# Kernel tuning notes

Measured on AMD Instinct MI355X. Metric: run time of the kernel, lower is better.

Reference implementation:

```python
import jax, jax.numpy as jnp
import numpy as np
import math

HEAD_DIM = 64
N_Q = 64
N_KV = 8
HIDDEN = 2880
SLIDING = 128
BASE = 150000.0
INIT_CTX = 4096
SCALE = 32.0
NTK_A = 1.0
NTK_B = 32.0
SEQ = 2048


def _rope_cos_sin(position_ids):
    # YaRN-scaled inverse frequencies (scaling_factor > 1 branch)
    freq = BASE ** (jnp.arange(0, HEAD_DIM, 2, dtype=jnp.float32) / HEAD_DIM)
    concentration = 0.1 * math.log(SCALE) + 1.0
    d_half = HEAD_DIM // 2
    low = d_half * math.log(INIT_CTX / (NTK_B * 2 * math.pi)) / math.log(BASE)
    high = d_half * math.log(INIT_CTX / (NTK_A * 2 * math.pi)) / math.log(BASE)
    interpolation = 1.0 / (SCALE * freq)
    extrapolation = 1.0 / freq
    ramp = (jnp.arange(d_half, dtype=jnp.float32) - low) / (high - low)
    mask = 1.0 - jnp.clip(ramp, 0.0, 1.0)
    inv_freq = interpolation * (1.0 - mask) + extrapolation * mask
    freqs = position_ids.astype(jnp.float32)[:, None] * inv_freq[None, :]  # [n, d/2]
    return jnp.cos(freqs) * concentration, jnp.sin(freqs) * concentration


def _apply_rope(x, cos, sin):
    # x: [n, h, d]; cos/sin: [n, d/2]
    cos = cos[:, None, :].astype(x.dtype)
    sin = sin[:, None, :].astype(x.dtype)
    x1, x2 = jnp.split(x, 2, axis=-1)
    return jnp.concatenate([x1 * cos - x2 * sin, x2 * cos + x1 * sin], axis=-1)


def setup_inputs() -> dict:
    key = jax.random.key(0)
    ks = jax.random.split(key, 6)
    qkv_dim = HEAD_DIM * (N_Q + 2 * N_KV)
    return {
        "hidden_states": jax.random.normal(ks[0], (SEQ, HIDDEN), dtype=jnp.float32),
        "qkv_w": jax.random.normal(ks[1], (qkv_dim, HIDDEN), dtype=jnp.float32) * 0.02,
        "qkv_b": jax.random.normal(ks[2], (qkv_dim,), dtype=jnp.float32) * 0.02,
        "o_w": jax.random.normal(ks[3], (HIDDEN, N_Q * HEAD_DIM), dtype=jnp.float32) * 0.02,
        "o_b": jax.random.normal(ks[4], (HIDDEN,), dtype=jnp.float32) * 0.02,
        "sinks": jax.random.normal(ks[5], (N_Q,), dtype=jnp.float32),
        "position_ids": jnp.arange(SEQ, dtype=jnp.int64 if jax.config.jax_enable_x64 else jnp.int32),
    }


def reference(hidden_states, qkv_w, qkv_b, o_w, o_b, sinks, position_ids):
    n = hidden_states.shape[0]
    scaling = HEAD_DIM ** (-0.5)

    # fused QKV projection + split
    qkv = hidden_states @ qkv_w.T + qkv_b  # [n, (nq+2*nkv)*d]
    q_sz, k_sz = N_Q * HEAD_DIM, N_KV * HEAD_DIM
    q = qkv[:, :q_sz].reshape(n, N_Q, HEAD_DIM)
    k = qkv[:, q_sz:q_sz + k_sz].reshape(n, N_KV, HEAD_DIM)
    v = qkv[:, q_sz + k_sz:].reshape(n, N_KV, HEAD_DIM)

    # RoPE (YaRN)
    cos, sin = _rope_cos_sin(position_ids)
    q = _apply_rope(q, cos, sin)
    k = _apply_rope(k, cos, sin)

    # GQA: repeat KV heads to match query heads
    groups = N_Q // N_KV
    k_full = jnp.repeat(k, groups, axis=1)  # [n, N_Q, d]
    v_full = jnp.repeat(v, groups, axis=1)

    scores = jnp.einsum('qhd,khd->hqk', q, k_full) * scaling  # [H, S, S]

    # sliding-window mask (distance > window -> -inf), as in source (no causal term)
    current_pos = position_ids.max()
    key_pos = current_pos - n + 1 + jnp.arange(n)
    dist = position_ids[:, None] - key_pos[None, :]
    win_mask = jnp.where(dist > SLIDING, -jnp.inf, 0.0).astype(scores.dtype)
    scores = scores + win_mask[None, :, :]

    # learned sink logit appended to softmax normalization
    sink = jnp.broadcast_to(sinks[:, None, None], (N_Q, n, 1)).astype(scores.dtype)
    logits = jnp.concatenate([scores, sink], axis=-1)  # [H, S, S+1]
    probs = jax.nn.softmax(logits, axis=-1)[..., :-1]   # drop sink column

    attn = jnp.einsum('hqk,khd->qhd', probs, v_full)    # [S, H, d]
    attn = attn.reshape(n, N_Q * HEAD_DIM)
    return attn @ o_w.T + o_b
```

## Files before the change

kernel.cpp:

```cpp
#include <hip/hip_runtime.h>
#include <hip/hip_bf16.h>
#include <stdint.h>

typedef __attribute__((ext_vector_type(4))) float f32x4;
typedef __attribute__((ext_vector_type(8))) short bf16x8;

#define SEQ 2048
#define HIDDEN 2880
#define NQ 64
#define NKV 8
#define HD 64
#define QKV_DIM 5120
#define Q_SZ 4096
#define K_SZ 512
#define OW_N 2880
#define OW_NPAD 2944
#define OW_K 4096

__device__ __forceinline__ unsigned short f2b_bits(float f) {
    unsigned int x = __float_as_uint(f);
    unsigned int r = (x + 0x7fffu + ((x >> 16) & 1u)) >> 16;
    return (unsigned short)r;
}
__device__ __forceinline__ float b2f(unsigned short u) {
    return __uint_as_float(((unsigned int)u) << 16);
}

__device__ __forceinline__ void llds16(const ushort* g, ushort* l) {
    __builtin_amdgcn_global_load_lds(
        (const __attribute__((address_space(1))) void*)g,
        (__attribute__((address_space(3))) void*)l, 16, 0, 0);
}

__global__ void convert_f32(const float* __restrict__ in, ushort* __restrict__ out, int n4) {
    int i = blockIdx.x * blockDim.x + threadIdx.x;
    int stride = gridDim.x * blockDim.x;
    for (; i < n4; i += stride) {
        float4 v = reinterpret_cast<const float4*>(in)[i];
        ushort4 o = make_ushort4(f2b_bits(v.x), f2b_bits(v.y), f2b_bits(v.z), f2b_bits(v.w));
        reinterpret_cast<ushort4*>(out)[i] = o;
    }
}

__global__ void convert_ow(const float* __restrict__ in, ushort* __restrict__ out) {
    int i = blockIdx.x * blockDim.x + threadIdx.x;
    const int n4 = OW_NPAD * OW_K / 4;
    int stride = gridDim.x * blockDim.x;
    for (; i < n4; i += stride) {
        int row = (i * 4) >> 12;
        ushort4 o;
        if (row < OW_N) {
            float4 v = reinterpret_cast<const float4*>(in)[i];
            o = make_ushort4(f2b_bits(v.x), f2b_bits(v.y), f2b_bits(v.z), f2b_bits(v.w));
        } else {
            o = make_ushort4(0, 0, 0, 0);
        }
        reinterpret_cast<ushort4*>(out)[i] = o;
    }
}

template<int OUT_BF16>
__global__ __launch_bounds__(256) void gemm_bt(
    const ushort* __restrict__ A, const ushort* __restrict__ B,
    const float* __restrict__ bias, void* __restrict__ Cout,
    int M, int N, int K, int Nreal, int ldC)
{
    __shared__ __align__(16) ushort As[128 * 64];
    __shared__ __align__(16) ushort Bs[128 * 64];
    const int tid = threadIdx.x;
    const int lane = tid & 63;
    const int w = tid >> 6;
    const int wr = w >> 1, wc = w & 1;
    const int m0 = blockIdx.y * 128, n0 = blockIdx.x * 128;

    f32x4 acc[4][4] = {};

    for (int k0 = 0; k0 < K; k0 += 64) {
        #pragma unroll
        for (int it = 0; it < 4; ++it) {
            int i = it * 256 + tid;
            int row = i >> 3;
            int col16 = (i ^ (row & 7)) & 7;
            const ushort* ga = A + (size_t)(m0 + row) * K + k0 + col16 * 8;
            ushort* la = As + (size_t)(it * 256 + (tid & ~63)) * 8;
            llds16(ga, la);
            const ushort* gb = B + (size_t)(n0 + row) * K + k0 + col16 * 8;
            ushort* lb = Bs + (size_t)(it * 256 + (tid & ~63)) * 8;
            llds16(gb, lb);
        }
        __syncthreads();
        #pragma unroll
        for (int kk = 0; kk < 2; ++kk) {
            bf16x8 a[4], b[4];
            #pragma unroll
            for (int mi = 0; mi < 4; ++mi) {
                int row = wr * 64 + mi * 16 + (lane & 15);
                int byte = row * 128 + kk * 64 + (lane >> 4) * 16;
                byte ^= (row & 7) << 4;
                a[mi] = *reinterpret_cast<const bf16x8*>(reinterpret_cast<const char*>(As) + byte);
            }
            #pragma unroll
            for (int ni = 0; ni < 4; ++ni) {
                int row = wc * 64 + ni * 16 + (lane & 15);
                int byte = row * 128 + kk * 64 + (lane >> 4) * 16;
                byte ^= (row & 7) << 4;
                b[ni] = *reinterpret_cast<const bf16x8*>(reinterpret_cast<const char*>(Bs) + byte);
            }
            #pragma unroll
            for (int mi = 0; mi < 4; ++mi)
                #pragma unroll
                for (int ni = 0; ni < 4; ++ni)
                    acc[mi][ni] = __builtin_amdgcn_mfma_f32_16x16x32_bf16(a[mi], b[ni], acc[mi][ni], 0, 0, 0);
        }
        __syncthreads();
    }

    #pragma unroll
    for (int mi = 0; mi < 4; ++mi) {
        int gr = m0 + wr * 64 + mi * 16 + (lane >> 4) * 4;
        #pragma unroll
        for (int ni = 0; ni < 4; ++ni) {
            int gc = n0 + wc * 64 + ni * 16 + (lane & 15);
            if (gc < Nreal) {
                float bv = bias[gc];
                #pragma unroll
                for (int r = 0; r < 4; ++r) {
                    float v = acc[mi][ni][r] + bv;
                    if (OUT_BF16)
                        ((ushort*)Cout)[(size_t)(gr + r) * ldC + gc] = f2b_bits(v);
                    else
                        ((float*)Cout)[(size_t)(gr + r) * ldC + gc] = v;
                }
            }
        }
    }
}

__global__ __launch_bounds__(256) void rope_kernel(
    const ushort* __restrict__ qkv, const int* __restrict__ pos,
    ushort* __restrict__ q_ro, ushort* __restrict__ k_ro)
{
    __shared__ float cosv[32], sinv[32];
    const int s = blockIdx.x;
    const int tid = threadIdx.x;
    if (tid < 32) {
        int j = tid;
        const float logbase = logf(150000.0f);
        float freq = expf((float)j * (logbase / 32.0f));
        float interp = 1.0f / (32.0f * freq);
        float extrap = 1.0f / freq;
        const float twopi = 6.283185307179586f;
        float low  = 32.0f * logf(4096.0f / (32.0f * twopi)) / logbase;
        float high = 32.0f * logf(4096.0f / (1.0f  * twopi)) / logbase;
        float ramp = ((float)j - low) / (high - low);
        float mask = 1.0f - fminf(fmaxf(ramp, 0.0f), 1.0f);
        float inv_freq = interp * (1.0f - mask) + extrap * mask;
        float ang = (float)pos[s] * inv_freq;
        const float conc = 0.1f * logf(32.0f) + 1.0f;
        cosv[j] = cosf(ang) * conc;
        sinv[j] = sinf(ang) * conc;
    }
    __syncthreads();
    const float qsc = 0.125f * 1.4426950408889634f;
    #pragma unroll
    for (int it = 0; it < 8; ++it) {
        int idx = it * 256 + tid;
        int h = idx >> 5, j = idx & 31;
        const ushort* src = qkv + (size_t)s * QKV_DIM + h * HD;
        float x1 = b2f(src[j]), x2 = b2f(src[j + 32]);
        float c = cosv[j], sn = sinv[j];
        ushort* dst = q_ro + ((size_t)h * SEQ + s) * HD;
        dst[j]      = f2b_bits((x1 * c - x2 * sn) * qsc);
        dst[j + 32] = f2b_bits((x2 * c + x1 * sn) * qsc);
    }
    {
        int h = tid >> 5, j = tid & 31;
        const ushort* src = qkv + (size_t)s * QKV_DIM + Q_SZ + h * HD;
        float x1 = b2f(src[j]), x2 = b2f(src[j + 32]);
        float c = cosv[j], sn = sinv[j];
        ushort* dst = k_ro + ((size_t)h * SEQ + s) * HD;
        dst[j]      = f2b_bits(x1 * c - x2 * sn);
        dst[j + 32] = f2b_bits(x2 * c + x1 * sn);
    }
}

__global__ __launch_bounds__(256) void vtrans_kernel(const ushort* __restrict__ qkv, ushort* __restrict__ vT) {
    __shared__ ushort t[64][65];
    const int kh = blockIdx.x >> 5;
    const int s0 = (blockIdx.x & 31) * 64;
    const int tid = threadIdx.x;
    #pragma unroll
    for (int it = 0; it < 16; ++it) {
        int e = it * 256 + tid;
        int sl = e >> 6, d = e & 63;
        t[d][sl] = qkv[(size_t)(s0 + sl) * QKV_DIM + Q_SZ + K_SZ + kh * HD + d];
    }
    __syncthreads();
    #pragma unroll
    for (int it = 0; it < 16; ++it) {
        int e = it * 256 + tid;
        int d = e >> 6, sl = e & 63;
        vT[((size_t)kh * HD + d) * SEQ + s0 + sl] = t[d][sl];
    }
}

__global__ __launch_bounds__(256, 4) void attn_kernel(
    const ushort* __restrict__ q_ro, const ushort* __restrict__ k_ro,
    const ushort* __restrict__ vT, const float* __restrict__ sinks,
    ushort* __restrict__ attn_out)
{
    __shared__ __align__(16) ushort Kb[2][4096];
    __shared__ __align__(16) ushort Vb[2][4096];
    __shared__ __align__(16) ushort Pl[4][1024];

    const int tid = threadIdx.x;
    const int lane = tid & 63;
    const int w = tid >> 6;
    const int l15 = lane & 15;
    const int l4 = lane >> 4;

    int wg = blockIdx.x;
    int wgid = (wg & 7) * 128 + (wg >> 3);
    const int kh = wgid >> 7;
    const int qh = (wgid >> 4) & 7;
    const int pp = wgid & 15;
    const int h = kh * 8 + qh;

    const float snk = sinks[h];
    char* pbase = (char*)&Pl[w][0];

    const short oneb = (short)0x3F80;
    const bf16x8 bones = {oneb, oneb, oneb, oneb, oneb, oneb, oneb, oneb};

    const int i0 = tid, i1 = 256 + tid;
    const int r0 = i0 >> 3, cs0 = (i0 ^ r0) & 7;
    const int r1 = i1 >> 3, cs1 = (i1 ^ r1) & 7;
    const ushort* gK0 = k_ro + (size_t)kh * (SEQ * 64) + r0 * 64 + cs0 * 8;
    const ushort* gK1 = k_ro + (size_t)kh * (SEQ * 64) + r1 * 64 + cs1 * 8;
    const ushort* gV0 = vT + ((size_t)kh * 64 + r0) * SEQ + cs0 * 8;
    const ushort* gV1 = vT + ((size_t)kh * 64 + r1) * SEQ + cs1 * 8;
    const int ld0 = (tid & ~63) * 8, ld1 = (256 + (tid & ~63)) * 8;

    const int swz = (l15 & 7) << 4;
    const int kvbase = l15 * 128 + ((l4 * 16) ^ swz);
    const int pwbase = l15 * 128 + ((l4 * 8) ^ swz);

    auto stage = [&](int bs, int k0) {
        llds16(gK0 + k0 * 64, &Kb[bs][ld0]);
        llds16(gK1 + k0 * 64, &Kb[bs][ld1]);
        llds16(gV0 + k0,      &Vb[bs][ld0]);
        llds16(gV1 + k0,      &Vb[bs][ld1]);
    };

    for (int sidx = 0; sidx < 2; ++sidx) {
        const int qt = sidx ? (31 - pp) : pp;
        const int q0 = qt * 64;
        const int qw = q0 + w * 16;

        bf16x8 aq[2];
        #pragma unroll
        for (int kc = 0; kc < 2; ++kc)
            aq[kc] = *reinterpret_cast<const bf16x8*>(
                q_ro + ((size_t)h * SEQ + qw + l15) * HD + kc * 32 + l4 * 8);

        f32x4 o[4] = {};
        f32x4 lacc = {0.f, 0.f, 0.f, 0.f};

        const int kt0 = (qt >= 2) ? (qt - 2) : 0;
        int cur = 0;

        stage(0, kt0 * 64);
        __syncthreads();

        for (int kt = kt0; kt < SEQ / 64; ++kt) {
            const int k0 = kt * 64;
            if (kt + 1 < SEQ / 64) stage(cur ^ 1, k0 + 64);

            f32x4 s[4];
            const f32x4 z = {0.f, 0.f, 0.f, 0.f};
            const char* kbp = (const char*)Kb[cur];
            __builtin_amdgcn_s_setprio(1);
            #pragma unroll
            for (int c = 0; c < 4; ++c) {
                bf16x8 bk0 = *reinterpret_cast<const bf16x8*>(kbp + c * 2048 + kvbase);
                s[c] = __builtin_amdgcn_mfma_f32_16x16x32_bf16(bk0, aq[0], z, 0, 0, 0);
                bf16x8 bk1 = *reinterpret_cast<const bf16x8*>(kbp + c * 2048 + (kvbase ^ 64));
                s[c] = __builtin_amdgcn_mfma_f32_16x16x32_bf16(bk1, aq[1], s[c], 0, 0, 0);
            }
            __builtin_amdgcn_s_setprio(0);

            if (k0 < qw - 113) {
                int thr = qw + l15 - 128 - k0;
                #pragma unroll
                for (int c = 0; c < 4; ++c)
                    #pragma unroll
                    for (int r = 0; r < 4; ++r)
                        if (c * 16 + l4 * 4 + r < thr) s[c][r] = -1e30f;
            }

            #pragma unroll
            for (int c = 0; c < 4; ++c) {
                float p0 = exp2f(s[c][0]), p1 = exp2f(s[c][1]);
                float p2 = exp2f(s[c][2]), p3 = exp2f(s[c][3]);
                unsigned int pk0, pk1;
                asm("v_cvt_pk_bf16_f32 %0, %1, %2" : "=v"(pk0) : "v"(p0), "v"(p1));
                asm("v_cvt_pk_bf16_f32 %0, %1, %2" : "=v"(pk1) : "v"(p2), "v"(p3));
                uint2 pv; pv.x = pk0; pv.y = pk1;
                *reinterpret_cast<uint2*>(pbase + (pwbase ^ (c * 32))) = pv;
            }

            const char* vbp = (const char*)Vb[cur];
            __builtin_amdgcn_s_setprio(1);
            #pragma unroll
            for (int kc = 0; kc < 2; ++kc) {
                bf16x8 pa = *reinterpret_cast<const bf16x8*>(pbase + (kvbase ^ (kc * 64)) - (kvbase & ~2047) + (l15 * 128 + ((l4 * 16) ^ swz) - l15 * 128));
                pa = *reinterpret_cast<const bf16x8*>(pbase + ((l15 * 128 + ((l4 * 16) ^ swz)) ^ (kc * 64)));
                lacc = __builtin_amdgcn_mfma_f32_16x16x32_bf16(pa, bones, lacc, 0, 0, 0);
                #pragma unroll
                for (int df = 0; df < 4; ++df) {
                    bf16x8 bv = *reinterpret_cast<const bf16x8*>(vbp + df * 2048 + (kvbase ^ (kc * 64)));
                    o[df] = __builtin_amdgcn_mfma_f32_16x16x32_bf16(pa, bv, o[df], 0, 0, 0);
                }
            }
            __builtin_amdgcn_s_setprio(0);

            __syncthreads();
            cur ^= 1;
        }

        {
            const float es = exp2f(snk * 1.4426950408889634f);
            float inv[4];
            #pragma unroll
            for (int r = 0; r < 4; ++r) inv[r] = 1.0f / (lacc[r] + es);
            #pragma unroll
            for (int df = 0; df < 4; ++df)
                #pragma unroll
                for (int r = 0; r < 4; ++r) {
                    int row = qw + l4 * 4 + r;
                    int col = df * 16 + l15;
                    attn_out[(size_t)row * Q_SZ + h * HD + col] = f2b_bits(o[df][r] * inv[r]);
                }
        }
    }
}

extern "C" void kernel_launch(void* const* d_in, const int* in_sizes, int n_in,
                              void* d_out, int out_size, void* d_ws, size_t ws_size,
                              hipStream_t stream) {
    const float* hidden = (const float*)d_in[0];
    const float* qkv_w  = (const float*)d_in[1];
    const float* qkv_b  = (const float*)d_in[2];
    const float* o_w    = (const float*)d_in[3];
    const float* o_b    = (const float*)d_in[4];
    const float* sinks  = (const float*)d_in[5];
    const int*   pos    = (const int*)d_in[6];
    float* out = (float*)d_out;

    char* ws = (char*)d_ws;
    size_t off = 0;
    auto alloc = [&](size_t bytes) {
        char* p = ws + off;
        off += (bytes + 255) & ~(size_t)255;
        return p;
    };
    ushort* hs_bf   = (ushort*)alloc((size_t)SEQ * HIDDEN * 2);
    ushort* wqkv_bf = (ushort*)alloc((size_t)QKV_DIM * HIDDEN * 2);
    ushort* qkv_bf  = (ushort*)alloc((size_t)SEQ * QKV_DIM * 2);
    ushort* q_ro    = (ushort*)alloc((size_t)NQ * SEQ * HD * 2);
    ushort* k_ro    = (ushort*)alloc((size_t)NKV * SEQ * HD * 2);
    ushort* vT      = (ushort*)alloc((size_t)NKV * HD * SEQ * 2);
    ushort* attn_bf = (ushort*)alloc((size_t)SEQ * Q_SZ * 2);
    ushort* wo_bf   = (ushort*)alloc((size_t)OW_NPAD * OW_K * 2);

    convert_f32<<<2048, 256, 0, stream>>>(hidden, hs_bf, SEQ * HIDDEN / 4);
    convert_f32<<<2048, 256, 0, stream>>>(qkv_w, wqkv_bf, QKV_DIM * HIDDEN / 4);
    convert_ow<<<2048, 256, 0, stream>>>(o_w, wo_bf);

    gemm_bt<1><<<dim3(QKV_DIM / 128, SEQ / 128), 256, 0, stream>>>(
        hs_bf, wqkv_bf, qkv_b, qkv_bf, SEQ, QKV_DIM, HIDDEN, QKV_DIM, QKV_DIM);

    rope_kernel<<<SEQ, 256, 0, stream>>>(qkv_bf, pos, q_ro, k_ro);
    vtrans_kernel<<<NKV * 32, 256, 0, stream>>>(qkv_bf, vT);

    attn_kernel<<<1024, 256, 0, stream>>>(q_ro, k_ro, vT, sinks, attn_bf);

    gemm_bt<0><<<dim3(OW_NPAD / 128, SEQ / 128), 256, 0, stream>>>(
        attn_bf, wo_bf, o_b, out, SEQ, OW_NPAD, OW_K, OW_N, OW_N);
}
```

Baseline: 275.2 us.

## Remap GEMM workgroups per XCD and merge the three conversion kernels

Both GEMMs now launch on a 1D grid. The block index is remapped so that workgroups landing on the same XCD (blockIdx mod 8) get consecutive tile ids. Those tiles walk down M for a fixed N column, so they share B-weight tiles in that chiplet's L2. The three fp32-to-bf16 conversion launches are folded into one kernel covering all three buffers, which saves launch overhead and tail gaps. A redundant, dead LDS load of the P fragment in the attention kernel is simplified into a single indexed load. The remap assumes the grid is divisible by 8 and that M has exactly 16 tiles.

Result: no change. 272.7 us (-0.9%).

```diff
diff --git a/kernel.cpp b/kernel.cpp
--- a/kernel.cpp
+++ b/kernel.cpp
@@ -32,30 +32,32 @@
         (__attribute__((address_space(3))) void*)l, 16, 0, 0);
 }
 
-__global__ void convert_f32(const float* __restrict__ in, ushort* __restrict__ out, int n4) {
+__global__ void convert_all(const float* __restrict__ hidden, const float* __restrict__ qkv_w,
+                            const float* __restrict__ o_w, ushort* __restrict__ hs_bf,
+                            ushort* __restrict__ wqkv_bf, ushort* __restrict__ wo_bf) {
+    const int N1 = SEQ * HIDDEN / 4;
+    const int N2 = N1 + QKV_DIM * HIDDEN / 4;
+    const int N3 = N2 + OW_NPAD * OW_K / 4;
     int i = blockIdx.x * blockDim.x + threadIdx.x;
     int stride = gridDim.x * blockDim.x;
-    for (; i < n4; i += stride) {
-        float4 v = reinterpret_cast<const float4*>(in)[i];
-        ushort4 o = make_ushort4(f2b_bits(v.x), f2b_bits(v.y), f2b_bits(v.z), f2b_bits(v.w));
-        reinterpret_cast<ushort4*>(out)[i] = o;
-    }
-}
-
-__global__ void convert_ow(const float* __restrict__ in, ushort* __restrict__ out) {
-    int i = blockIdx.x * blockDim.x + threadIdx.x;
-    const int n4 = OW_NPAD * OW_K / 4;
-    int stride = gridDim.x * blockDim.x;
-    for (; i < n4; i += stride) {
-        int row = (i * 4) >> 12;
-        ushort4 o;
-        if (row < OW_N) {
-            float4 v = reinterpret_cast<const float4*>(in)[i];
-            o = make_ushort4(f2b_bits(v.x), f2b_bits(v.y), f2b_bits(v.z), f2b_bits(v.w));
+    for (; i < N3; i += stride) {
+        const float* src;
+        ushort* dst;
+        int j;
+        if (i < N1) {
+            j = i; src = hidden; dst = hs_bf;
+        } else if (i < N2) {
+            j = i - N1; src = qkv_w; dst = wqkv_bf;
         } else {
-            o = make_ushort4(0, 0, 0, 0);
-        }
-        reinterpret_cast<ushort4*>(out)[i] = o;
+            j = i - N2; src = o_w; dst = wo_bf;
+            if ((j >> 10) >= OW_N) {
+                reinterpret_cast<ushort4*>(dst)[j] = make_ushort4(0, 0, 0, 0);
+                continue;
+            }
+        }
+        float4 v = reinterpret_cast<const float4*>(src)[j];
+        reinterpret_cast<ushort4*>(dst)[j] =
+            make_ushort4(f2b_bits(v.x), f2b_bits(v.y), f2b_bits(v.z), f2b_bits(v.w));
     }
 }
 
@@ -71,7 +73,12 @@
     const int lane = tid & 63;
     const int w = tid >> 6;
     const int wr = w >> 1, wc = w & 1;
-    const int m0 = blockIdx.y * 128, n0 = blockIdx.x * 128;
+
+    const int nwg = gridDim.x;
+    const int per = nwg >> 3;
+    const int wgid = (blockIdx.x & 7) * per + (blockIdx.x >> 3);
+    const int m0 = (wgid & 15) * 128;
+    const int n0 = (wgid >> 4) * 128;
 
     f32x4 acc[4][4] = {};
 
@@ -313,8 +320,7 @@
             __builtin_amdgcn_s_setprio(1);
             #pragma unroll
             for (int kc = 0; kc < 2; ++kc) {
-                bf16x8 pa = *reinterpret_cast<const bf16x8*>(pbase + (kvbase ^ (kc * 64)) - (kvbase & ~2047) + (l15 * 128 + ((l4 * 16) ^ swz) - l15 * 128));
-                pa = *reinterpret_cast<const bf16x8*>(pbase + ((l15 * 128 + ((l4 * 16) ^ swz)) ^ (kc * 64)));
+                bf16x8 pa = *reinterpret_cast<const bf16x8*>(pbase + (kvbase ^ (kc * 64)));
                 lacc = __builtin_amdgcn_mfma_f32_16x16x32_bf16(pa, bones, lacc, 0, 0, 0);
                 #pragma unroll
                 for (int df = 0; df < 4; ++df) {
@@ -373,11 +379,9 @@
     ushort* attn_bf = (ushort*)alloc((size_t)SEQ * Q_SZ * 2);
     ushort* wo_bf   = (ushort*)alloc((size_t)OW_NPAD * OW_K * 2);
 
-    convert_f32<<<2048, 256, 0, stream>>>(hidden, hs_bf, SEQ * HIDDEN / 4);
-    convert_f32<<<2048, 256, 0, stream>>>(qkv_w, wqkv_bf, QKV_DIM * HIDDEN / 4);
-    convert_ow<<<2048, 256, 0, stream>>>(o_w, wo_bf);
-
-    gemm_bt<1><<<dim3(QKV_DIM / 128, SEQ / 128), 256, 0, stream>>>(
+    convert_all<<<2048, 256, 0, stream>>>(hidden, qkv_w, o_w, hs_bf, wqkv_bf, wo_bf);
+
+    gemm_bt<1><<<(QKV_DIM / 128) * (SEQ / 128), 256, 0, stream>>>(
         hs_bf, wqkv_bf, qkv_b, qkv_bf, SEQ, QKV_DIM, HIDDEN, QKV_DIM, QKV_DIM);
 
     rope_kernel<<<SEQ, 256, 0, stream>>>(qkv_bf, pos, q_ro, k_ro);
@@ -385,6 +389,6 @@
 
     attn_kernel<<<1024, 256, 0, stream>>>(q_ro, k_ro, vT, sinks, attn_bf);
 
-    gemm_bt<0><<<dim3(OW_NPAD / 128, SEQ / 128), 256, 0, stream>>>(
+    gemm_bt<0><<<(OW_NPAD / 128) * (SEQ / 128), 256, 0, stream>>>(
         attn_bf, wo_bf, o_b, out, SEQ, OW_NPAD, OW_K, OW_N, OW_N);
 }
```
